# Performance work log

Measured on AMD Instinct MI355X. Metric: run time of the kernel, lower is better.

The kernel has to match this reference:

```python
import jax, jax.numpy as jnp
import numpy as np

FEAT_DIM = 256
HEAD_DIM = 32
N_HEADS = FEAT_DIM // HEAD_DIM
SIZE = 8  # sqrt(max_seq_len)
P = SIZE * SIZE  # 64
B, G = 4, 1024


def _rel_pos_index(size: int) -> np.ndarray:
    coords = np.stack(np.meshgrid(np.arange(size), np.arange(size), indexing='ij'))
    flat = coords.reshape(2, -1)
    rel = flat[:, :, None] - flat[:, None, :]
    rel = rel.transpose(1, 2, 0).copy()
    rel[:, :, 0] += size - 1
    rel[:, :, 1] += size - 1
    rel[:, :, 0] *= 2 * size - 1
    return rel.sum(-1)  # [P, P], values in [0, (2*size-1)^2)


def setup_inputs() -> dict:
    key = jax.random.key(0)
    ks = jax.random.split(key, 6)
    d = FEAT_DIM
    w_std = d ** -0.5
    return {
        'x': jax.random.normal(ks[0], (B, G, P, d), dtype=jnp.float32),
        'Wqkv': jax.random.normal(ks[1], (d, 3 * d), dtype=jnp.float32) * w_std,
        'bqkv': jnp.zeros((3 * d,), dtype=jnp.float32),
        'Wm': jax.random.normal(ks[2], (d, d), dtype=jnp.float32) * w_std,
        'bm': jnp.zeros((d,), dtype=jnp.float32),
        'bias_table': jax.random.normal(ks[3], ((2 * SIZE - 1) ** 2, N_HEADS), dtype=jnp.float32) * 0.02,
        'rel_index': jnp.asarray(_rel_pos_index(SIZE), dtype=jnp.int32),
    }


def reference(x, Wqkv, bqkv, Wm, bm, bias_table, rel_index):
    Bb, Gg, Pp, D = x.shape
    H, DH = N_HEADS, HEAD_DIM
    scale = D ** -0.5  # note: scale uses feat_dim, as in the original
    qkv = x @ Wqkv + bqkv  # [B,G,P,3D]
    q, k, v = jnp.split(qkv, 3, axis=-1)
    q = q.reshape(Bb, Gg, Pp, H, DH)
    k = k.reshape(Bb, Gg, Pp, H, DH) * scale
    v = v.reshape(Bb, Gg, Pp, H, DH)
    scores = jnp.einsum('BGIHD,BGJHD->BGHIJ', q, k)  # [B,G,H,P,P]
    # gathered relative-position bias: [P,P,H] -> [1,1,H,P,P]
    bias = bias_table[rel_index]  # [P,P,H]
    bias = jnp.transpose(bias, (2, 0, 1))[None, None]  # [1,1,H,P,P]
    attn = jax.nn.softmax(scores + bias, axis=-1)
    out = jnp.einsum('BGHIJ,BGJHD->BGIHD', attn, v)
    out = out.reshape(Bb, Gg, Pp, D)
    return out @ Wm + bm
```

## Files before the change

### kernel.cpp

```cpp
#include <hip/hip_runtime.h>
#include <hip/hip_bf16.h>

typedef short short8 __attribute__((ext_vector_type(8)));
typedef float f32x4 __attribute__((ext_vector_type(4)));

#define XB_OFF 0
#define SCR_OFF 16896
#define LDS_TOT 37376
#define STX 264
#define ST40 40
#define ST72 72

static __device__ __forceinline__ unsigned short f2b(float f) {
  union { float f; unsigned u; } v; v.f = f;
  unsigned r = v.u + 0x7FFFu + ((v.u >> 16) & 1u);
  return (unsigned short)(r >> 16);
}
static __device__ __forceinline__ unsigned pk2(float a, float b) {
  union { __hip_bfloat162 h; unsigned u; } v;
  v.h = __float22bfloat162_rn(make_float2(a, b));
  return v.u;
}

__global__ void prep_w_kernel(const float* __restrict__ W, unsigned short* __restrict__ Wf,
                              int ncols, int total, int qkv) {
  const int tid = blockIdx.x * blockDim.x + threadIdx.x;
  if (tid >= total) return;
  const int l  = tid & 63;
  const int ks = (tid >> 6) & 7;
  const int nt = tid >> 9;
  int col;
  if (qkv) {
    const int wv = nt / 6, tt = nt % 6;
    col = (tt >> 1) * 256 + wv * 32 + (tt & 1) * 16 + (l & 15);
  } else {
    col = nt * 16 + (l & 15);
  }
  const int k0 = ks * 32 + (l >> 4) * 8;
  short8 v;
#pragma unroll
  for (int j = 0; j < 8; ++j) v[j] = (short)f2b(W[(size_t)(k0 + j) * ncols + col]);
  *reinterpret_cast<short8*>(&Wf[(size_t)tid * 8]) = v;
}

__global__ void prep_bias_kernel(const float* __restrict__ bt, const int* __restrict__ ri,
                                 float* __restrict__ bc) {
  const int tid = blockIdx.x * blockDim.x + threadIdx.x;
  if (tid >= 8192) return;
  const int l  = tid & 63;
  const int t  = (tid >> 6) & 15;
  const int h  = tid >> 10;
  const int mt = t >> 2, nt = t & 3;
  f32x4 v;
#pragma unroll
  for (int i = 0; i < 4; ++i) {
    const int r = mt * 16 + (l >> 4) * 4 + i;
    const int c = nt * 16 + (l & 15);
    v[i] = bt[ri[c * 64 + r] * 8 + h];
  }
  *reinterpret_cast<f32x4*>(&bc[(size_t)tid * 4]) = v;
}

__global__ __launch_bounds__(512, 4)
void win_attn_kernel(const float* __restrict__ x,
                     const float* __restrict__ bqkv,
                     const float* __restrict__ bm,
                     const unsigned short* __restrict__ Wqkv_f,
                     const unsigned short* __restrict__ Wm_f,
                     const float* __restrict__ bias_c,
                     float* __restrict__ out)
{
  __shared__ unsigned short sm[LDS_TOT];
  const int tid = threadIdx.x;
  const int w   = tid >> 6;
  const int l   = tid & 63;
  const int lr  = l & 15;
  const int lg  = l >> 4;
  const long long win = blockIdx.x;
  const float* xw = x + win * 16384;
  const int SW = SCR_OFF + w * 2560;

#pragma unroll
  for (int it = 0; it < 8; ++it) {
    const int f = it * 2048 + tid * 4;
    const int row = f >> 8, col = f & 255;
    const float4 v = *reinterpret_cast<const float4*>(xw + f);
    *reinterpret_cast<uint2*>(&sm[XB_OFF + row * STX + col]) =
        make_uint2(pk2(v.x, v.y), pk2(v.z, v.w));
  }
  __syncthreads();

  short8 qf[4], kf[4], vf[2][2];
#pragma unroll
  for (int m = 0; m < 3; ++m) {
    f32x4 acc[4][2];
    {
      const float bb0 = bqkv[m * 256 + w * 32 + lr];
      const float bb1 = bqkv[m * 256 + w * 32 + 16 + lr];
#pragma unroll
      for (int mt = 0; mt < 4; ++mt) {
        acc[mt][0] = (f32x4){bb0, bb0, bb0, bb0};
        acc[mt][1] = (f32x4){bb1, bb1, bb1, bb1};
      }
    }
#pragma unroll
    for (int ks = 0; ks < 8; ++ks) {
      short8 a[4];
#pragma unroll
      for (int mt = 0; mt < 4; ++mt)
        a[mt] = *reinterpret_cast<const short8*>(
            &sm[XB_OFF + (lr + 16 * mt) * STX + lg * 8 + ks * 32]);
      __builtin_amdgcn_s_setprio(1);
#pragma unroll
      for (int sub = 0; sub < 2; ++sub) {
        const short8 bf = *reinterpret_cast<const short8*>(
            &Wqkv_f[(size_t)(((w * 6 + m * 2 + sub) * 8 + ks) * 64 + l) * 8]);
#pragma unroll
        for (int mt = 0; mt < 4; ++mt)
          acc[mt][sub] = __builtin_amdgcn_mfma_f32_16x16x32_bf16(a[mt], bf, acc[mt][sub], 0, 0, 0);
      }
      __builtin_amdgcn_s_setprio(0);
    }

    if (m == 2) {
#pragma unroll
      for (int sub = 0; sub < 2; ++sub)
#pragma unroll
        for (int mt = 0; mt < 4; ++mt)
          *reinterpret_cast<uint2*>(&sm[SW + (sub * 16 + lr) * ST72 + 16 * mt + 4 * lg]) =
              make_uint2(pk2(acc[mt][sub][0], acc[mt][sub][1]),
                         pk2(acc[mt][sub][2], acc[mt][sub][3]));
#pragma unroll
      for (int nt = 0; nt < 2; ++nt)
#pragma unroll
        for (int kh = 0; kh < 2; ++kh)
          vf[nt][kh] = *reinterpret_cast<const short8*>(
              &sm[SW + (lr + 16 * nt) * ST72 + kh * 32 + lg * 8]);
    } else {
      const float sc = (m == 1) ? 0.0625f : 1.0f;
#pragma unroll
      for (int sub = 0; sub < 2; ++sub)
#pragma unroll
        for (int mt = 0; mt < 4; ++mt) {
          const unsigned p01 = pk2(acc[mt][sub][0] * sc, acc[mt][sub][1] * sc);
          const unsigned p23 = pk2(acc[mt][sub][2] * sc, acc[mt][sub][3] * sc);
          const int b = SW + (16 * mt + 4 * lg) * ST40 + sub * 16 + lr;
          sm[b]            = (unsigned short)p01;
          sm[b + ST40]     = (unsigned short)(p01 >> 16);
          sm[b + 2 * ST40] = (unsigned short)p23;
          sm[b + 3 * ST40] = (unsigned short)(p23 >> 16);
        }
#pragma unroll
      for (int mt = 0; mt < 4; ++mt) {
        const short8 fr = *reinterpret_cast<const short8*>(
            &sm[SW + (lr + 16 * mt) * ST40 + lg * 8]);
        if (m == 0) qf[mt] = fr; else kf[mt] = fr;
      }
    }
  }

  f32x4 s[4][4];
  __builtin_amdgcn_s_setprio(1);
#pragma unroll
  for (int mt = 0; mt < 4; ++mt)
#pragma unroll
    for (int nt = 0; nt < 4; ++nt) {
      const f32x4 bb = *reinterpret_cast<const f32x4*>(
          &bias_c[(size_t)((w * 16 + mt * 4 + nt) * 64 + l) * 4]);
      s[mt][nt] = __builtin_amdgcn_mfma_f32_16x16x32_bf16(kf[mt], qf[nt], bb, 0, 0, 0);
    }
  __builtin_amdgcn_s_setprio(0);

  float rs[4];
#pragma unroll
  for (int nt = 0; nt < 4; ++nt) {
    float m01 = fmaxf(fmaxf(s[0][nt][0], s[0][nt][1]), fmaxf(s[0][nt][2], s[0][nt][3]));
    float m23 = fmaxf(fmaxf(s[1][nt][0], s[1][nt][1]), fmaxf(s[1][nt][2], s[1][nt][3]));
    float m45 = fmaxf(fmaxf(s[2][nt][0], s[2][nt][1]), fmaxf(s[2][nt][2], s[2][nt][3]));
    float m67 = fmaxf(fmaxf(s[3][nt][0], s[3][nt][1]), fmaxf(s[3][nt][2], s[3][nt][3]));
    float mx = fmaxf(fmaxf(m01, m23), fmaxf(m45, m67));
    mx = fmaxf(mx, __shfl_xor(mx, 16));
    mx = fmaxf(mx, __shfl_xor(mx, 32));
    float sum = 0.f;
#pragma unroll
    for (int mt = 0; mt < 4; ++mt)
#pragma unroll
      for (int i = 0; i < 4; ++i) {
        const float e = __expf(s[mt][nt][i] - mx);
        s[mt][nt][i] = e;
        sum += e;
      }
    sum += __shfl_xor(sum, 16);
    sum += __shfl_xor(sum, 32);
    rs[nt] = 1.0f / sum;
  }

  f32x4 o[4][2];
#pragma unroll
  for (int mt = 0; mt < 4; ++mt)
#pragma unroll
    for (int nt = 0; nt < 2; ++nt) o[mt][nt] = (f32x4){0.f, 0.f, 0.f, 0.f};
#pragma unroll
  for (int kh = 0; kh < 2; ++kh) {
#pragma unroll
    for (int mtl = 0; mtl < 2; ++mtl)
#pragma unroll
      for (int nt = 0; nt < 4; ++nt) {
        const int mt = 2 * kh + mtl;
        *reinterpret_cast<uint2*>(&sm[SW + (lr + 16 * nt) * ST40 + mtl * 16 + 4 * lg]) =
            make_uint2(pk2(s[mt][nt][0] * rs[nt], s[mt][nt][1] * rs[nt]),
                       pk2(s[mt][nt][2] * rs[nt], s[mt][nt][3] * rs[nt]));
      }
    __builtin_amdgcn_s_setprio(1);
#pragma unroll
    for (int mt = 0; mt < 4; ++mt) {
      const short8 pa = *reinterpret_cast<const short8*>(
          &sm[SW + (lr + 16 * mt) * ST40 + lg * 8]);
#pragma unroll
      for (int nt = 0; nt < 2; ++nt)
        o[mt][nt] = __builtin_amdgcn_mfma_f32_16x16x32_bf16(pa, vf[nt][kh], o[mt][nt], 0, 0, 0);
    }
    __builtin_amdgcn_s_setprio(0);
  }

  __syncthreads();
#pragma unroll
  for (int mt = 0; mt < 4; ++mt)
#pragma unroll
    for (int nt = 0; nt < 2; ++nt) {
      const unsigned p01 = pk2(o[mt][nt][0], o[mt][nt][1]);
      const unsigned p23 = pk2(o[mt][nt][2], o[mt][nt][3]);
      const int b = XB_OFF + (16 * mt + 4 * lg) * STX + w * 32 + nt * 16 + lr;
      sm[b]           = (unsigned short)p01;
      sm[b + STX]     = (unsigned short)(p01 >> 16);
      sm[b + 2 * STX] = (unsigned short)p23;
      sm[b + 3 * STX] = (unsigned short)(p23 >> 16);
    }
  __syncthreads();

  f32x4 po[4][2];
  {
    const float bm0 = bm[w * 32 + lr];
    const float bm1 = bm[w * 32 + 16 + lr];
#pragma unroll
    for (int mt = 0; mt < 4; ++mt) {
      po[mt][0] = (f32x4){bm0, bm0, bm0, bm0};
      po[mt][1] = (f32x4){bm1, bm1, bm1, bm1};
    }
  }
#pragma unroll
  for (int ks = 0; ks < 8; ++ks) {
    short8 a[4];
#pragma unroll
    for (int mt = 0; mt < 4; ++mt)
      a[mt] = *reinterpret_cast<const short8*>(
          &sm[XB_OFF + (lr + 16 * mt) * STX + lg * 8 + ks * 32]);
    __builtin_amdgcn_s_setprio(1);
#pragma unroll
    for (int nt = 0; nt < 2; ++nt) {
      const short8 bf = *reinterpret_cast<const short8*>(
          &Wm_f[(size_t)(((w * 2 + nt) * 8 + ks) * 64 + l) * 8]);
#pragma unroll
      for (int mt = 0; mt < 4; ++mt)
        po[mt][nt] = __builtin_amdgcn_mfma_f32_16x16x32_bf16(a[mt], bf, po[mt][nt], 0, 0, 0);
    }
    __builtin_amdgcn_s_setprio(0);
  }

  float* ow = out + win * 16384;
#pragma unroll
  for (int mt = 0; mt < 4; ++mt)
#pragma unroll
    for (int nt = 0; nt < 2; ++nt)
#pragma unroll
      for (int i = 0; i < 4; ++i)
        ow[(16 * mt + 4 * lg + i) * 256 + w * 32 + nt * 16 + lr] = po[mt][nt][i];
}

extern "C" void kernel_launch(void* const* d_in, const int* in_sizes, int n_in,
                              void* d_out, int out_size, void* d_ws, size_t ws_size,
                              hipStream_t stream) {
  const float* x    = (const float*)d_in[0];
  const float* Wqkv = (const float*)d_in[1];
  const float* bqkv = (const float*)d_in[2];
  const float* Wm   = (const float*)d_in[3];
  const float* bm   = (const float*)d_in[4];
  const float* bt   = (const float*)d_in[5];
  const int*   ri   = (const int*)d_in[6];

  unsigned short* Wqkv_f = (unsigned short*)d_ws;
  unsigned short* Wm_f   = (unsigned short*)((char*)d_ws + 393216);
  float*          bias_c = (float*)((char*)d_ws + 524288);

  prep_w_kernel<<<48, 512, 0, stream>>>(Wqkv, Wqkv_f, 768, 24576, 1);
  prep_w_kernel<<<16, 512, 0, stream>>>(Wm, Wm_f, 256, 8192, 0);
  prep_bias_kernel<<<16, 512, 0, stream>>>(bt, ri, bias_c);

  const int nwin = in_sizes[0] / 16384;
  win_attn_kernel<<<nwin, 512, 0, stream>>>(x, bqkv, bm, Wqkv_f, Wm_f, bias_c, (float*)d_out);
}
```

Baseline: 246.0 us.

## Shrink per-wave LDS scratch and process attention per query tile to raise occupancy

Halves the per-wave LDS scratch region by staging Q/K/V fragments in two halves and streaming softmax and PV per query tile instead of holding the full 4x4 score tile. This lowers register and LDS use so launch bounds can ask for 6 blocks per CU instead of 4, aiming to hide latency better. The cost is an extra barrier before the score phase, more LDS round trips in smaller chunks, and possible register spills under the tighter bound.

```diff
diff --git a/kernel.cpp b/kernel.cpp
--- a/kernel.cpp
+++ b/kernel.cpp
@@ -6,7 +6,7 @@
 
 #define XB_OFF 0
 #define SCR_OFF 16896
-#define LDS_TOT 37376
+#define LDS_TOT 27136
 #define STX 264
 #define ST40 40
 #define ST72 72
@@ -61,7 +61,7 @@
   *reinterpret_cast<f32x4*>(&bc[(size_t)tid * 4]) = v;
 }
 
-__global__ __launch_bounds__(512, 4)
+__global__ __launch_bounds__(512, 6)
 void win_attn_kernel(const float* __restrict__ x,
                      const float* __restrict__ bqkv,
                      const float* __restrict__ bm,
@@ -78,7 +78,7 @@
   const int lg  = l >> 4;
   const long long win = blockIdx.x;
   const float* xw = x + win * 16384;
-  const int SW = SCR_OFF + w * 2560;
+  const int SW = SCR_OFF + w * 1280;
 
 #pragma unroll
   for (int it = 0; it < 8; ++it) {
@@ -124,60 +124,66 @@
 
     if (m == 2) {
 #pragma unroll
-      for (int sub = 0; sub < 2; ++sub)
-#pragma unroll
-        for (int mt = 0; mt < 4; ++mt)
-          *reinterpret_cast<uint2*>(&sm[SW + (sub * 16 + lr) * ST72 + 16 * mt + 4 * lg]) =
-              make_uint2(pk2(acc[mt][sub][0], acc[mt][sub][1]),
-                         pk2(acc[mt][sub][2], acc[mt][sub][3]));
-#pragma unroll
-      for (int nt = 0; nt < 2; ++nt)
-#pragma unroll
-        for (int kh = 0; kh < 2; ++kh)
+      for (int kh = 0; kh < 2; ++kh) {
+#pragma unroll
+        for (int sub = 0; sub < 2; ++sub)
+#pragma unroll
+          for (int mtl = 0; mtl < 2; ++mtl) {
+            const int mt = 2 * kh + mtl;
+            *reinterpret_cast<uint2*>(&sm[SW + (sub * 16 + lr) * ST40 + 16 * mtl + 4 * lg]) =
+                make_uint2(pk2(acc[mt][sub][0], acc[mt][sub][1]),
+                           pk2(acc[mt][sub][2], acc[mt][sub][3]));
+          }
+#pragma unroll
+        for (int nt = 0; nt < 2; ++nt)
           vf[nt][kh] = *reinterpret_cast<const short8*>(
-              &sm[SW + (lr + 16 * nt) * ST72 + kh * 32 + lg * 8]);
+              &sm[SW + (lr + 16 * nt) * ST40 + lg * 8]);
+      }
     } else {
       const float sc = (m == 1) ? 0.0625f : 1.0f;
 #pragma unroll
-      for (int sub = 0; sub < 2; ++sub)
-#pragma unroll
-        for (int mt = 0; mt < 4; ++mt) {
-          const unsigned p01 = pk2(acc[mt][sub][0] * sc, acc[mt][sub][1] * sc);
-          const unsigned p23 = pk2(acc[mt][sub][2] * sc, acc[mt][sub][3] * sc);
-          const int b = SW + (16 * mt + 4 * lg) * ST40 + sub * 16 + lr;
-          sm[b]            = (unsigned short)p01;
-          sm[b + ST40]     = (unsigned short)(p01 >> 16);
-          sm[b + 2 * ST40] = (unsigned short)p23;
-          sm[b + 3 * ST40] = (unsigned short)(p23 >> 16);
+      for (int th = 0; th < 2; ++th) {
+#pragma unroll
+        for (int sub = 0; sub < 2; ++sub)
+#pragma unroll
+          for (int mtl = 0; mtl < 2; ++mtl) {
+            const int mt = 2 * th + mtl;
+            const unsigned p01 = pk2(acc[mt][sub][0] * sc, acc[mt][sub][1] * sc);
+            const unsigned p23 = pk2(acc[mt][sub][2] * sc, acc[mt][sub][3] * sc);
+            const int b = SW + (16 * mtl + 4 * lg) * ST40 + sub * 16 + lr;
+            sm[b]            = (unsigned short)p01;
+            sm[b + ST40]     = (unsigned short)(p01 >> 16);
+            sm[b + 2 * ST40] = (unsigned short)p23;
+            sm[b + 3 * ST40] = (unsigned short)(p23 >> 16);
+          }
+#pragma unroll
+        for (int tl = 0; tl < 2; ++tl) {
+          const short8 fr = *reinterpret_cast<const short8*>(
+              &sm[SW + (lr + 16 * tl) * ST40 + lg * 8]);
+          if (m == 0) qf[2 * th + tl] = fr; else kf[2 * th + tl] = fr;
         }
-#pragma unroll
-      for (int mt = 0; mt < 4; ++mt) {
-        const short8 fr = *reinterpret_cast<const short8*>(
-            &sm[SW + (lr + 16 * mt) * ST40 + lg * 8]);
-        if (m == 0) qf[mt] = fr; else kf[mt] = fr;
-      }
-    }
-  }
-
-  f32x4 s[4][4];
-  __builtin_amdgcn_s_setprio(1);
-#pragma unroll
-  for (int mt = 0; mt < 4; ++mt)
-#pragma unroll
-    for (int nt = 0; nt < 4; ++nt) {
+      }
+    }
+  }
+
+  __syncthreads();
+
+#pragma unroll
+  for (int nt = 0; nt < 4; ++nt) {
+    f32x4 sq[4];
+    __builtin_amdgcn_s_setprio(1);
+#pragma unroll
+    for (int mt = 0; mt < 4; ++mt) {
       const f32x4 bb = *reinterpret_cast<const f32x4*>(
           &bias_c[(size_t)((w * 16 + mt * 4 + nt) * 64 + l) * 4]);
-      s[mt][nt] = __builtin_amdgcn_mfma_f32_16x16x32_bf16(kf[mt], qf[nt], bb, 0, 0, 0);
-    }
-  __builtin_amdgcn_s_setprio(0);
-
-  float rs[4];
-#pragma unroll
-  for (int nt = 0; nt < 4; ++nt) {
-    float m01 = fmaxf(fmaxf(s[0][nt][0], s[0][nt][1]), fmaxf(s[0][nt][2], s[0][nt][3]));
-    float m23 = fmaxf(fmaxf(s[1][nt][0], s[1][nt][1]), fmaxf(s[1][nt][2], s[1][nt][3]));
-    float m45 = fmaxf(fmaxf(s[2][nt][0], s[2][nt][1]), fmaxf(s[2][nt][2], s[2][nt][3]));
-    float m67 = fmaxf(fmaxf(s[3][nt][0], s[3][nt][1]), fmaxf(s[3][nt][2], s[3][nt][3]));
+      sq[mt] = __builtin_amdgcn_mfma_f32_16x16x32_bf16(kf[mt], qf[nt], bb, 0, 0, 0);
+    }
+    __builtin_amdgcn_s_setprio(0);
+
+    float m01 = fmaxf(fmaxf(sq[0][0], sq[0][1]), fmaxf(sq[0][2], sq[0][3]));
+    float m23 = fmaxf(fmaxf(sq[1][0], sq[1][1]), fmaxf(sq[1][2], sq[1][3]));
+    float m45 = fmaxf(fmaxf(sq[2][0], sq[2][1]), fmaxf(sq[2][2], sq[2][3]));
+    float m67 = fmaxf(fmaxf(sq[3][0], sq[3][1]), fmaxf(sq[3][2], sq[3][3]));
     float mx = fmaxf(fmaxf(m01, m23), fmaxf(m45, m67));
     mx = fmaxf(mx, __shfl_xor(mx, 16));
     mx = fmaxf(mx, __shfl_xor(mx, 32));
@@ -186,56 +192,43 @@
     for (int mt = 0; mt < 4; ++mt)
 #pragma unroll
       for (int i = 0; i < 4; ++i) {
-        const float e = __expf(s[mt][nt][i] - mx);
-        s[mt][nt][i] = e;
+        const float e = __expf(sq[mt][i] - mx);
+        sq[mt][i] = e;
         sum += e;
       }
     sum += __shfl_xor(sum, 16);
     sum += __shfl_xor(sum, 32);
-    rs[nt] = 1.0f / sum;
-  }
-
-  f32x4 o[4][2];
-#pragma unroll
-  for (int mt = 0; mt < 4; ++mt)
-#pragma unroll
-    for (int nt = 0; nt < 2; ++nt) o[mt][nt] = (f32x4){0.f, 0.f, 0.f, 0.f};
-#pragma unroll
-  for (int kh = 0; kh < 2; ++kh) {
-#pragma unroll
-    for (int mtl = 0; mtl < 2; ++mtl)
-#pragma unroll
-      for (int nt = 0; nt < 4; ++nt) {
-        const int mt = 2 * kh + mtl;
-        *reinterpret_cast<uint2*>(&sm[SW + (lr + 16 * nt) * ST40 + mtl * 16 + 4 * lg]) =
-            make_uint2(pk2(s[mt][nt][0] * rs[nt], s[mt][nt][1] * rs[nt]),
-                       pk2(s[mt][nt][2] * rs[nt], s[mt][nt][3] * rs[nt]));
-      }
-    __builtin_amdgcn_s_setprio(1);
-#pragma unroll
-    for (int mt = 0; mt < 4; ++mt) {
+    const float rs = 1.0f / sum;
+
+#pragma unroll
+    for (int mt = 0; mt < 4; ++mt)
+      *reinterpret_cast<uint2*>(&sm[SW + lr * ST72 + mt * 16 + 4 * lg]) =
+          make_uint2(pk2(sq[mt][0] * rs, sq[mt][1] * rs),
+                     pk2(sq[mt][2] * rs, sq[mt][3] * rs));
+
+    f32x4 oq[2] = {(f32x4){0.f, 0.f, 0.f, 0.f}, (f32x4){0.f, 0.f, 0.f, 0.f}};
+#pragma unroll
+    for (int kh = 0; kh < 2; ++kh) {
       const short8 pa = *reinterpret_cast<const short8*>(
-          &sm[SW + (lr + 16 * mt) * ST40 + lg * 8]);
-#pragma unroll
-      for (int nt = 0; nt < 2; ++nt)
-        o[mt][nt] = __builtin_amdgcn_mfma_f32_16x16x32_bf16(pa, vf[nt][kh], o[mt][nt], 0, 0, 0);
-    }
-    __builtin_amdgcn_s_setprio(0);
-  }
-
-  __syncthreads();
-#pragma unroll
-  for (int mt = 0; mt < 4; ++mt)
-#pragma unroll
-    for (int nt = 0; nt < 2; ++nt) {
-      const unsigned p01 = pk2(o[mt][nt][0], o[mt][nt][1]);
-      const unsigned p23 = pk2(o[mt][nt][2], o[mt][nt][3]);
-      const int b = XB_OFF + (16 * mt + 4 * lg) * STX + w * 32 + nt * 16 + lr;
+          &sm[SW + lr * ST72 + kh * 32 + lg * 8]);
+      __builtin_amdgcn_s_setprio(1);
+#pragma unroll
+      for (int ntd = 0; ntd < 2; ++ntd)
+        oq[ntd] = __builtin_amdgcn_mfma_f32_16x16x32_bf16(pa, vf[ntd][kh], oq[ntd], 0, 0, 0);
+      __builtin_amdgcn_s_setprio(0);
+    }
+
+#pragma unroll
+    for (int ntd = 0; ntd < 2; ++ntd) {
+      const unsigned p01 = pk2(oq[ntd][0], oq[ntd][1]);
+      const unsigned p23 = pk2(oq[ntd][2], oq[ntd][3]);
+      const int b = XB_OFF + (nt * 16 + 4 * lg) * STX + w * 32 + ntd * 16 + lr;
       sm[b]           = (unsigned short)p01;
       sm[b + STX]     = (unsigned short)(p01 >> 16);
       sm[b + 2 * STX] = (unsigned short)p23;
       sm[b + 3 * STX] = (unsigned short)(p23 >> 16);
     }
+  }
   __syncthreads();
 
   f32x4 po[4][2];
```

Measured after the change: 425.7 us. 1.73x slower.
